# Kernel tuning notes

Hardware: AMD Instinct MI355X
Metric: run time of the kernel (lower is better)

The kernel has to match this reference:

```python
import jax, jax.numpy as jnp
import numpy as np

B, T, C = 8, 2048, 1024


def setup_inputs() -> dict:
    key = jax.random.key(0)
    ks = jax.random.split(key, 7)
    s = 0.02  # typical init scale for weights
    return {
        "x": jax.random.normal(ks[0], (B, T, C), jnp.float32),
        "wq": jax.random.normal(ks[1], (C, C), jnp.float32) * s,
        "bq": jax.random.normal(ks[2], (C,), jnp.float32) * s,
        "wk": jax.random.normal(ks[3], (C, C), jnp.float32) * s,
        "bk": jax.random.normal(ks[4], (C,), jnp.float32) * s,
        "wv": jax.random.normal(ks[5], (C, C), jnp.float32) * s,
        "bv": jax.random.normal(ks[6], (C,), jnp.float32) * s,
    }


def reference(x, wq, bq, wk, bk, wv, bv):
    # x: [B, T, C]; torch Linear stores weight as [out, in] -> x @ W.T + b
    Bx, Tx, Cx = x.shape
    Q = x @ wq.T + bq  # [B, T, C]
    K = x @ wk.T + bk
    V = x @ wv.T + bv
    # NOTE: source computes K @ Q^T (keys index rows, queries index columns)
    scores = jnp.einsum("btc,bsc->bts", K, Q) / jnp.sqrt(jnp.float32(Cx))  # [B, T, T]
    causal = jnp.tril(jnp.ones((Tx, Tx), dtype=bool))  # mask==0 above diagonal
    scores = jnp.where(causal, scores, -jnp.inf)
    # torch masked_fill with a (1,1,T,T) mask broadcasts scores to (1,B,T,T)
    scores = scores[None]  # [1, B, T, T]
    w = jax.nn.softmax(scores, axis=-1)
    out = jnp.einsum("abts,bsc->abtc", w, V)  # [1, B, T, C]
    return out
```

## Files before the change

### kernel.cpp

```cpp
#include <hip/hip_runtime.h>
#include <stdint.h>

typedef unsigned short u16;
typedef __attribute__((ext_vector_type(8))) __bf16 bf16x8;
typedef __attribute__((ext_vector_type(4))) float f32x4;

#define DEVI __device__ __forceinline__

DEVI u16 f32_to_bf16(float f) {
  uint32_t u = __builtin_bit_cast(uint32_t, f);
  u += 0x7FFFu + ((u >> 16) & 1u);
  return (u16)(u >> 16);
}

DEVI void gl2lds16(const void* g, void* l) {
  __builtin_amdgcn_global_load_lds(
      (const __attribute__((address_space(1))) void*)g,
      (__attribute__((address_space(3))) void*)l, 16, 0, 0);
}

#define SMEM_U16 17408

#define S_BATCH 2228224

DEVI void gemm_bt_mainloop(const u16* __restrict__ A, const u16* __restrict__ B,
                           int lda, int ldb, int kIters,
                           u16* As, u16* Bs, f32x4 (&acc)[4][4]) {
  const int tid = threadIdx.x;
  const int lane = tid & 63;
  const int wid = tid >> 6;
  const int wr = wid >> 1, wc = wid & 1;
  const int l15 = lane & 15, quad = lane >> 4;

  const int srow = tid >> 3;
  const int sgrp = ((tid & 7) - srow) & 7;
  const u16* Ag = A + (size_t)srow * lda + sgrp * 8;
  const u16* Bg = B + (size_t)srow * ldb + sgrp * 8;
  char* AsDst = (char*)As + tid * 16;
  char* BsDst = (char*)Bs + tid * 16;

  const int a_row0 = wr * 64 + l15;
  const int b_row0 = wc * 64 + l15;

  for (int kb = 0; kb < kIters; ++kb) {
#pragma unroll
    for (int r = 0; r < 4; ++r) {
      gl2lds16(Ag + (size_t)(r * 32) * lda, AsDst + r * 4096);
      gl2lds16(Bg + (size_t)(r * 32) * ldb, BsDst + r * 4096);
    }
    Ag += 64;
    Bg += 64;
    __syncthreads();
#pragma unroll
    for (int kk = 0; kk < 2; ++kk) {
      const int gA = ((kk * 4 + quad + a_row0) & 7) * 8;
      const int gB = ((kk * 4 + quad + b_row0) & 7) * 8;
      bf16x8 af[4], bfr[4];
#pragma unroll
      for (int i = 0; i < 4; ++i)
        af[i] = *(const bf16x8*)(As + (a_row0 + i * 16) * 64 + gA);
#pragma unroll
      for (int j = 0; j < 4; ++j)
        bfr[j] = *(const bf16x8*)(Bs + (b_row0 + j * 16) * 64 + gB);
#pragma unroll
      for (int i = 0; i < 4; ++i)
#pragma unroll
        for (int j = 0; j < 4; ++j)
          acc[i][j] = __builtin_amdgcn_mfma_f32_16x16x32_bf16(af[i], bfr[j],
                                                              acc[i][j], 0, 0, 0);
    }
    __syncthreads();
  }
}

DEVI void store_tile_bf16(const u16* tile, u16* __restrict__ out, int ld_out) {
  const int tid = threadIdx.x;
  const int c0 = (tid & 15) * 8;
#pragma unroll
  for (int rr = 0; rr < 8; ++rr) {
    const int row = rr * 16 + (tid >> 4);
    const uint4 v = *(const uint4*)(tile + row * 136 + c0);
    *(uint4*)(out + (size_t)row * ld_out + c0) = v;
  }
}

__global__ void cast_f32_to_bf16_kernel(const float* __restrict__ src,
                                        u16* __restrict__ dst, int n4) {
  int i = blockIdx.x * blockDim.x + threadIdx.x;
  const int stride = gridDim.x * blockDim.x;
  for (; i < n4; i += stride) {
    const float4 v = ((const float4*)src)[i];
    ushort4 o;
    o.x = f32_to_bf16(v.x);
    o.y = f32_to_bf16(v.y);
    o.z = f32_to_bf16(v.z);
    o.w = f32_to_bf16(v.w);
    ((ushort4*)dst)[i] = o;
  }
}

__global__ void cast_w_kernel(const float* __restrict__ wq,
                              const float* __restrict__ wk,
                              const float* __restrict__ wv,
                              u16* __restrict__ wb, float* __restrict__ sums) {
  const int z = blockIdx.y;
  if (z == 3) {
    int i = blockIdx.x * blockDim.x + threadIdx.x;
    if (i < 4096) ((float4*)sums)[i] = (float4){0.f, 0.f, 0.f, 0.f};
    return;
  }
  const float* src = (z == 0) ? wq : (z == 1) ? wk : wv;
  u16* dst = wb + (size_t)z * 1048576;
  int i = blockIdx.x * blockDim.x + threadIdx.x;
  const int stride = gridDim.x * blockDim.x;
  for (; i < 262144; i += stride) {
    const float4 v = ((const float4*)src)[i];
    ushort4 o;
    o.x = f32_to_bf16(v.x);
    o.y = f32_to_bf16(v.y);
    o.z = f32_to_bf16(v.z);
    o.w = f32_to_bf16(v.w);
    ((ushort4*)dst)[i] = o;
  }
}

__global__ __launch_bounds__(512, 2) void qkv_kernel(
    const u16* __restrict__ xb, const u16* __restrict__ wb,
    const float* __restrict__ bq, const float* __restrict__ bk,
    const float* __restrict__ bv, u16* __restrict__ Qb, u16* __restrict__ Kb,
    u16* __restrict__ Vt) {
  __shared__ __align__(16) u16 lds[65536];

  const int id = blockIdx.x;
  const int wg = (id & 7) * 96 + (id >> 3);
  const int g = wg >> 3, u = wg & 7;
  const int z = g >> 5;
  const int tp = g & 31;
  const int tmt = tp * 2 + (u >> 2);
  const int tct = u & 3;

  int m0, n0;
  const u16* Aptr;
  const u16* Bptr;
  if (z < 2) {
    m0 = tct * 256;
    n0 = tmt * 256;
    Aptr = wb + (size_t)z * 1048576 + (size_t)m0 * 1024;
    Bptr = xb + (size_t)n0 * 1024;
  } else {
    m0 = tmt * 256;
    n0 = tct * 256;
    Aptr = xb + (size_t)m0 * 1024;
    Bptr = wb + (size_t)2 * 1048576 + (size_t)n0 * 1024;
  }

  const int tid = threadIdx.x;
  const int srow = tid >> 3;
  const int sgrp = ((tid & 7) - srow) & 7;
  const u16* Ag = Aptr + (size_t)srow * 1024 + sgrp * 8;
  const u16* Bg = Bptr + (size_t)srow * 1024 + sgrp * 8;
  char* ldsDst = (char*)lds + tid * 16;

#define ST_A0(kt) do { const u16* s_ = Ag + (kt) * 64;           char* d_ = ldsDst + (((kt) & 1) * 65536);         gl2lds16(s_, d_); gl2lds16(s_ + 65536, d_ + 8192); } while (0)
#define ST_A1(kt) do { const u16* s_ = Ag + 131072 + (kt) * 64;  char* d_ = ldsDst + (((kt) & 1) * 65536) + 16384; gl2lds16(s_, d_); gl2lds16(s_ + 65536, d_ + 8192); } while (0)
#define ST_B0(kt) do { const u16* s_ = Bg + (kt) * 64;           char* d_ = ldsDst + (((kt) & 1) * 65536) + 32768; gl2lds16(s_, d_); gl2lds16(s_ + 65536, d_ + 8192); } while (0)
#define ST_B1(kt) do { const u16* s_ = Bg + 131072 + (kt) * 64;  char* d_ = ldsDst + (((kt) & 1) * 65536) + 49152; gl2lds16(s_, d_); gl2lds16(s_ + 65536, d_ + 8192); } while (0)

  ST_A0(0); ST_B0(0); ST_B1(0); ST_A1(0);
  ST_A0(1); ST_B0(1); ST_B1(1);

  const int lane = tid & 63, wid = tid >> 6;
  const int wr = wid >> 2, wc = wid & 3;
  const int l15 = lane & 15, quad = lane >> 4;

  int aoff[4][2], boff[2][2];
#pragma unroll
  for (int i_ = 0; i_ < 4; ++i_) {
    const int arow = wr * 64 + i_ * 16 + l15;
#pragma unroll
    for (int k_ = 0; k_ < 2; ++k_)
      aoff[i_][k_] = arow * 64 + ((k_ * 4 + quad + arow) & 7) * 8;
  }
#pragma unroll
  for (int j_ = 0; j_ < 2; ++j_) {
    const int brow = wc * 32 + j_ * 16 + l15;
#pragma unroll
    for (int k_ = 0; k_ < 2; ++k_)
      boff[j_][k_] = brow * 64 + ((k_ * 4 + quad + brow) & 7) * 8;
  }

  f32x4 acc[2][2][4][2];
#pragma unroll
  for (int a_ = 0; a_ < 2; ++a_)
#pragma unroll
    for (int b_ = 0; b_ < 2; ++b_)
#pragma unroll
      for (int i_ = 0; i_ < 4; ++i_)
#pragma unroll
        for (int j_ = 0; j_ < 2; ++j_)
          acc[a_][b_][i_][j_] = (f32x4){0.f, 0.f, 0.f, 0.f};

  bf16x8 af[4][2], bfr[2][2][2];

#define LOADA(qm, buf) do { const u16* p_ = lds + (buf) * 32768 + (qm) * 8192; \
  _Pragma("unroll") for (int i_ = 0; i_ < 4; ++i_) \
  _Pragma("unroll") for (int k_ = 0; k_ < 2; ++k_) \
    af[i_][k_] = *(const bf16x8*)(p_ + aoff[i_][k_]); } while (0)
#define LOADB(qn, buf) do { const u16* p_ = lds + (buf) * 32768 + 16384 + (qn) * 8192; \
  _Pragma("unroll") for (int j_ = 0; j_ < 2; ++j_) \
  _Pragma("unroll") for (int k_ = 0; k_ < 2; ++k_) \
    bfr[qn][j_][k_] = *(const bf16x8*)(p_ + boff[j_][k_]); } while (0)
#define MMA(qm, qn) do { \
  _Pragma("unroll") for (int i_ = 0; i_ < 4; ++i_) \
  _Pragma("unroll") for (int j_ = 0; j_ < 2; ++j_) \
  _Pragma("unroll") for (int k_ = 0; k_ < 2; ++k_) \
    acc[qm][qn][i_][j_] = __builtin_amdgcn_mfma_f32_16x16x32_bf16( \
        af[i_][k_], bfr[qn][j_][k_], acc[qm][qn][i_][j_], 0, 0, 0); } while (0)

#define BAR __builtin_amdgcn_s_barrier()
#define WLG0 asm volatile("s_waitcnt lgkmcnt(0)")
#define WLG8 asm volatile("s_waitcnt lgkmcnt(8)")
#define PRIO1 __builtin_amdgcn_s_setprio(1)
#define PRIO0 __builtin_amdgcn_s_setprio(0)

  asm volatile("s_waitcnt vmcnt(6)" ::: "memory");
  BAR;

#pragma unroll 1
  for (int it = 0; it < 7; ++it) {
    const int j0 = 2 * it;
    LOADA(0, 0); LOADB(0, 0); ST_A1(j0 + 1); WLG8;
    BAR; WLG0; PRIO1; MMA(0, 0); PRIO0; BAR;
    LOADB(1, 0); ST_A0(j0 + 2);
    BAR; WLG0; PRIO1; MMA(0, 1); PRIO0; BAR;
    LOADA(1, 0); ST_B0(j0 + 2);
    BAR; WLG0; PRIO1; MMA(1, 1); PRIO0; BAR;
    ST_B1(j0 + 2);
    BAR; PRIO1; MMA(1, 0); PRIO0;
    asm volatile("s_waitcnt vmcnt(6)" ::: "memory");
    BAR;
    LOADA(0, 1); LOADB(0, 1); ST_A1(j0 + 2); WLG8;
    BAR; WLG0; PRIO1; MMA(0, 0); PRIO0; BAR;
    LOADB(1, 1); ST_A0(j0 + 3);
    BAR; WLG0; PRIO1; MMA(0, 1); PRIO0; BAR;
    LOADA(1, 1); ST_B0(j0 + 3);
    BAR; WLG0; PRIO1; MMA(1, 1); PRIO0; BAR;
    ST_B1(j0 + 3);
    BAR; PRIO1; MMA(1, 0); PRIO0;
    asm volatile("s_waitcnt vmcnt(6)" ::: "memory");
    BAR;
  }
  {
    LOADA(0, 0); LOADB(0, 0); ST_A1(15); WLG8;
    BAR; WLG0; PRIO1; MMA(0, 0); PRIO0; BAR;
    LOADB(1, 0);
    BAR; WLG0; PRIO1; MMA(0, 1); PRIO0; BAR;
    LOADA(1, 0);
    BAR; WLG0; PRIO1; MMA(1, 1); PRIO0; BAR;
    PRIO1; MMA(1, 0); PRIO0;
    asm volatile("s_waitcnt vmcnt(0)" ::: "memory");
    BAR;
    LOADA(0, 1); LOADB(0, 1); WLG8;
    BAR; WLG0; PRIO1; MMA(0, 0); PRIO0; BAR;
    LOADB(1, 1);
    BAR; WLG0; PRIO1; MMA(0, 1); PRIO0; BAR;
    LOADA(1, 1);
    BAR; WLG0; PRIO1; MMA(1, 1); PRIO0; BAR;
    PRIO1; MMA(1, 0); PRIO0;
    BAR;
  }

  if (z < 2) {
    const float* bias = (z == 0) ? bq : bk;
    u16* Out = (z == 0) ? Qb : Kb;
#pragma unroll
    for (int th = 0; th < 2; ++th) {
      if (th) __syncthreads();
#pragma unroll
      for (int qm = 0; qm < 2; ++qm)
#pragma unroll
        for (int i_ = 0; i_ < 4; ++i_) {
          const int c = qm * 128 + wr * 64 + i_ * 16 + quad * 4;
          const float4 b4 = *(const float4*)(bias + m0 + c);
#pragma unroll
          for (int j_ = 0; j_ < 2; ++j_) {
            const int row = wc * 32 + j_ * 16 + l15;
            ushort4 o;
            o.x = f32_to_bf16(acc[qm][th][i_][j_][0] + b4.x);
            o.y = f32_to_bf16(acc[qm][th][i_][j_][1] + b4.y);
            o.z = f32_to_bf16(acc[qm][th][i_][j_][2] + b4.z);
            o.w = f32_to_bf16(acc[qm][th][i_][j_][3] + b4.w);
            *(ushort4*)(lds + row * 264 + c) = o;
          }
        }
      __syncthreads();
#pragma unroll
      for (int p = 0; p < 8; ++p) {
        const int row = p * 16 + (tid >> 5);
        const int c0 = (tid & 31) * 8;
        const uint4 v = *(const uint4*)(lds + row * 264 + c0);
        *(uint4*)(Out + (size_t)(n0 + th * 128 + row) * 1024 + m0 + c0) = v;
      }
    }
  } else {
    const int b = m0 >> 11;
    const int t0b = m0 & 2047;
    u16* Out = Vt + (size_t)b * 2097152;
#pragma unroll
    for (int th = 0; th < 2; ++th) {
      if (th) __syncthreads();
#pragma unroll
      for (int j_ = 0; j_ < 2; ++j_) {
        const int row = wc * 32 + j_ * 16 + l15;
        const float bb = bv[n0 + th * 128 + row];
#pragma unroll
        for (int qm = 0; qm < 2; ++qm)
#pragma unroll
          for (int i_ = 0; i_ < 4; ++i_) {
            const int c = qm * 128 + wr * 64 + i_ * 16 + quad * 4;
            ushort4 o;
            o.x = f32_to_bf16(acc[qm][th][i_][j_][0] + bb);
            o.y = f32_to_bf16(acc[qm][th][i_][j_][1] + bb);
            o.z = f32_to_bf16(acc[qm][th][i_][j_][2] + bb);
            o.w = f32_to_bf16(acc[qm][th][i_][j_][3] + bb);
            *(ushort4*)(lds + row * 264 + c) = o;
          }
      }
      __syncthreads();
#pragma unroll
      for (int p = 0; p < 8; ++p) {
        const int row = p * 16 + (tid >> 5);
        const int c0 = (tid & 31) * 8;
        const uint4 v = *(const uint4*)(lds + row * 264 + c0);
        *(uint4*)(Out + (size_t)(n0 + th * 128 + row) * 2048 + t0b + c0) = v;
      }
    }
  }
#undef ST_A0
#undef ST_A1
#undef ST_B0
#undef ST_B1
#undef LOADA
#undef LOADB
#undef MMA
#undef BAR
#undef WLG0
#undef WLG8
#undef PRIO1
#undef PRIO0
}

__global__ __launch_bounds__(256) void score_kernel(const u16* __restrict__ Kb,
                                                    const u16* __restrict__ Qb,
                                                    u16* __restrict__ Spk,
                                                    float* __restrict__ sums) {
  const int b = blockIdx.x & 7;
  const int l = 135 - (blockIdx.x >> 3);
  int rt = (int)((sqrtf(8.f * l + 1.f) - 1.f) * 0.5f);
  int ct = l - rt * (rt + 1) / 2;
  if (ct > rt) { ++rt; ct = l - rt * (rt + 1) / 2; }
  if (ct < 0)  { --rt; ct = l - rt * (rt + 1) / 2; }

  __shared__ __align__(16) u16 smem[SMEM_U16];
  u16* As = smem;
  u16* Bs = smem + 8192;

  f32x4 acc[4][4];
#pragma unroll
  for (int i = 0; i < 4; ++i)
#pragma unroll
    for (int j = 0; j < 4; ++j) acc[i][j] = (f32x4){0.f, 0.f, 0.f, 0.f};

  const u16* A = Qb + ((size_t)b * 2048 + ct * 128) * 1024;
  const u16* B = Kb + ((size_t)b * 2048 + rt * 128) * 1024;
  gemm_bt_mainloop(A, B, 1024, 1024, 16, As, Bs, acc);

  const int tid = threadIdx.x;
  const int lane = tid & 63, wid = tid >> 6;
  const int wr = wid >> 1, wc = wid & 1;
  const int l15 = lane & 15, quad = lane >> 4;
  const bool diag = (rt == ct);

  float sj[4] = {0.f, 0.f, 0.f, 0.f};
#pragma unroll
  for (int i = 0; i < 4; ++i) {
    const int s0 = wr * 64 + i * 16 + quad * 4;
#pragma unroll
    for (int j = 0; j < 4; ++j) {
      const int t = wc * 64 + j * 16 + l15;
      ushort4 o;
      float e[4];
#pragma unroll
      for (int r = 0; r < 4; ++r) {
        float v = __expf(acc[i][j][r] * 0.03125f);
        if (diag && (s0 + r) > t) v = 0.f;
        e[r] = v;
        sj[j] += v;
      }
      o.x = f32_to_bf16(e[0]);
      o.y = f32_to_bf16(e[1]);
      o.z = f32_to_bf16(e[2]);
      o.w = f32_to_bf16(e[3]);
      *(ushort4*)(smem + t * 136 + s0) = o;
    }
  }
#pragma unroll
  for (int j = 0; j < 4; ++j) {
    float v = sj[j];
    v += __shfl_xor(v, 16);
    v += __shfl_xor(v, 32);
    if (quad == 0)
      atomicAdd(&sums[(size_t)b * 2048 + rt * 128 + wc * 64 + j * 16 + l15], v);
  }
  __syncthreads();
  const int ld = (rt + 1) * 128;
  u16* Out = Spk + (size_t)b * S_BATCH + (size_t)(rt * (rt + 1) / 2) * 16384 +
             ct * 128;
  store_tile_bf16(smem, Out, ld);
}

__global__ __launch_bounds__(256) void pv_kernel(const u16* __restrict__ Spk,
                                                 const u16* __restrict__ Vt,
                                                 const float* __restrict__ sums,
                                                 float* __restrict__ Out) {
  const int b = blockIdx.x & 7;
  const int local = 127 - (blockIdx.x >> 3);
  const int rt = local >> 3;
  const int ct = local & 7;

  __shared__ __align__(16) u16 smem[SMEM_U16];
  u16* As = smem;
  u16* Bs = smem + 8192;
  float* ftile = (float*)smem;

  f32x4 acc[4][4];
#pragma unroll
  for (int i = 0; i < 4; ++i)
#pragma unroll
    for (int j = 0; j < 4; ++j) acc[i][j] = (f32x4){0.f, 0.f, 0.f, 0.f};

  const u16* A = Vt + ((size_t)b * 1024 + ct * 128) * 2048;
  const u16* B = Spk + (size_t)b * S_BATCH +
                 (size_t)(rt * (rt + 1) / 2) * 16384;
  const int ldb = (rt + 1) * 128;
  gemm_bt_mainloop(A, B, 2048, ldb, (rt + 1) * 2, As, Bs, acc);

  const int tid = threadIdx.x;
  const int lane = tid & 63, wid = tid >> 6;
  const int wr = wid >> 1, wc = wid & 1;
  const int l15 = lane & 15, quad = lane >> 4;

  const float* sumsb = sums + (size_t)b * 2048 + rt * 128;
  float* Ob = Out + (size_t)b * 2048 * 1024 + (size_t)(rt * 128) * 1024 +
              ct * 128;
#pragma unroll
  for (int h = 0; h < 2; ++h) {
    if (wc == h) {
#pragma unroll
      for (int j = 0; j < 4; ++j) {
        const int tl = j * 16 + l15;
        const float iv = 1.0f / sumsb[h * 64 + tl];
#pragma unroll
        for (int i = 0; i < 4; ++i) {
          const int c0 = wr * 64 + i * 16 + quad * 4;
          float4 v;
          v.x = acc[i][j][0] * iv;
          v.y = acc[i][j][1] * iv;
          v.z = acc[i][j][2] * iv;
          v.w = acc[i][j][3] * iv;
          *(float4*)(ftile + tl * 132 + c0) = v;
        }
      }
    }
    __syncthreads();
#pragma unroll
    for (int rr = 0; rr < 8; ++rr) {
      const int row = rr * 8 + (tid >> 5);
      const int c0 = (tid & 31) * 4;
      const float4 v = *(const float4*)(ftile + row * 132 + c0);
      *(float4*)(Ob + (size_t)(h * 64 + row) * 1024 + c0) = v;
    }
    __syncthreads();
  }
}

extern "C" void kernel_launch(void* const* d_in, const int* in_sizes, int n_in,
                              void* d_out, int out_size, void* d_ws,
                              size_t ws_size, hipStream_t stream) {
  const float* x = (const float*)d_in[0];
  const float* wq = (const float*)d_in[1];
  const float* bq = (const float*)d_in[2];
  const float* wk = (const float*)d_in[3];
  const float* bk = (const float*)d_in[4];
  const float* wv = (const float*)d_in[5];
  const float* bv = (const float*)d_in[6];
  float* out = (float*)d_out;
  char* ws = (char*)d_ws;

  u16* Qb = (u16*)(ws);
  u16* Kb = (u16*)(ws + ((size_t)32 << 20));
  u16* Vt = (u16*)(ws + ((size_t)64 << 20));
  u16* Spk = (u16*)(ws + ((size_t)96 << 20));
  u16* xb = (u16*)(ws + ((size_t)96 << 20));
  float* sums = (float*)(ws + ((size_t)132 << 20));
  u16* wb = (u16*)(ws + ((size_t)134 << 20));

  cast_f32_to_bf16_kernel<<<16384, 256, 0, stream>>>(x, xb, 16777216 / 4);
  cast_w_kernel<<<dim3(512, 4), 256, 0, stream>>>(wq, wk, wv, wb, sums);

  qkv_kernel<<<768, 512, 0, stream>>>(xb, wb, bq, bk, bv, Qb, Kb, Vt);

  score_kernel<<<8 * 136, 256, 0, stream>>>(Kb, Qb, Spk, sums);

  pv_kernel<<<8 * 128, 256, 0, stream>>>(Spk, Vt, sums, out);
}
```

Before: 337.7 us.

## Rewrite score kernel with 256x128 tiles and pipelined LDS loads

The score kernel moves from 128x128 tiles with 256 threads to 256x128 tiles (256 query rows by 128 key rows) with 512 threads. It reuses the qkv kernel's double-buffered global_load_lds pipeline with setprio and interleaved barriers, and the tile enumeration is remapped so that diagonal tiles are half-masked. The qkv mainloop also reorders its LDS fragment loads to run right after each MMA phase instead of before the barrier, dropping the partial lgkmcnt waits. The aim is better operand reuse and fewer blocks for the score GEMM. The cost is that partially masked half tiles still compute their full 256 columns, and the larger LDS footprint lowers occupancy.

```diff
diff --git a/kernel.cpp b/kernel.cpp
--- a/kernel.cpp
+++ b/kernel.cpp
@@ -70,17 +70,6 @@
                                                               acc[i][j], 0, 0, 0);
     }
     __syncthreads();
-  }
-}
-
-DEVI void store_tile_bf16(const u16* tile, u16* __restrict__ out, int ld_out) {
-  const int tid = threadIdx.x;
-  const int c0 = (tid & 15) * 8;
-#pragma unroll
-  for (int rr = 0; rr < 8; ++rr) {
-    const int row = rr * 16 + (tid >> 4);
-    const uint4 v = *(const uint4*)(tile + row * 136 + c0);
-    *(uint4*)(out + (size_t)row * ld_out + c0) = v;
   }
 }
 
@@ -219,55 +208,51 @@
 
 #define BAR __builtin_amdgcn_s_barrier()
 #define WLG0 asm volatile("s_waitcnt lgkmcnt(0)")
-#define WLG8 asm volatile("s_waitcnt lgkmcnt(8)")
 #define PRIO1 __builtin_amdgcn_s_setprio(1)
 #define PRIO0 __builtin_amdgcn_s_setprio(0)
-
-  asm volatile("s_waitcnt vmcnt(6)" ::: "memory");
+#define WVM6 asm volatile("s_waitcnt vmcnt(6)" ::: "memory")
+#define WVM0 asm volatile("s_waitcnt vmcnt(0)" ::: "memory")
+
+  WVM6;
   BAR;
 
 #pragma unroll 1
   for (int it = 0; it < 7; ++it) {
     const int j0 = 2 * it;
-    LOADA(0, 0); LOADB(0, 0); ST_A1(j0 + 1); WLG8;
-    BAR; WLG0; PRIO1; MMA(0, 0); PRIO0; BAR;
-    LOADB(1, 0); ST_A0(j0 + 2);
-    BAR; WLG0; PRIO1; MMA(0, 1); PRIO0; BAR;
-    LOADA(1, 0); ST_B0(j0 + 2);
+    LOADA(0, 0); LOADB(0, 0); ST_A1(j0 + 1);
+    BAR; WLG0; PRIO1; MMA(0, 0); PRIO0; LOADB(1, 0); BAR;
+    ST_A0(j0 + 2);
+    BAR; WLG0; PRIO1; MMA(0, 1); PRIO0; LOADA(1, 0); BAR;
+    ST_B0(j0 + 2);
     BAR; WLG0; PRIO1; MMA(1, 1); PRIO0; BAR;
     ST_B1(j0 + 2);
     BAR; PRIO1; MMA(1, 0); PRIO0;
-    asm volatile("s_waitcnt vmcnt(6)" ::: "memory");
+    WVM6;
     BAR;
-    LOADA(0, 1); LOADB(0, 1); ST_A1(j0 + 2); WLG8;
-    BAR; WLG0; PRIO1; MMA(0, 0); PRIO0; BAR;
-    LOADB(1, 1); ST_A0(j0 + 3);
-    BAR; WLG0; PRIO1; MMA(0, 1); PRIO0; BAR;
-    LOADA(1, 1); ST_B0(j0 + 3);
+    LOADA(0, 1); LOADB(0, 1); ST_A1(j0 + 2);
+    BAR; WLG0; PRIO1; MMA(0, 0); PRIO0; LOADB(1, 1); BAR;
+    ST_A0(j0 + 3);
+    BAR; WLG0; PRIO1; MMA(0, 1); PRIO0; LOADA(1, 1); BAR;
+    ST_B0(j0 + 3);
     BAR; WLG0; PRIO1; MMA(1, 1); PRIO0; BAR;
     ST_B1(j0 + 3);
     BAR; PRIO1; MMA(1, 0); PRIO0;
-    asm volatile("s_waitcnt vmcnt(6)" ::: "memory");
+    WVM6;
     BAR;
   }
   {
-    LOADA(0, 0); LOADB(0, 0); ST_A1(15); WLG8;
-    BAR; WLG0; PRIO1; MMA(0, 0); PRIO0; BAR;
-    LOADB(1, 0);
-    BAR; WLG0; PRIO1; MMA(0, 1); PRIO0; BAR;
-    LOADA(1, 0);
+    LOADA(0, 0); LOADB(0, 0); ST_A1(15);
+    BAR; WLG0; PRIO1; MMA(0, 0); PRIO0; LOADB(1, 0); BAR;
+    BAR; WLG0; PRIO1; MMA(0, 1); PRIO0; LOADA(1, 0); BAR;
+    BAR; WLG0; PRIO1; MMA(1, 1); PRIO0; BAR;
+    BAR; PRIO1; MMA(1, 0); PRIO0;
+    WVM0;
+    BAR;
+    LOADA(0, 1); LOADB(0, 1);
+    BAR; WLG0; PRIO1; MMA(0, 0); PRIO0; LOADB(1, 1); BAR;
+    BAR; WLG0; PRIO1; MMA(0, 1); PRIO0; LOADA(1, 1); BAR;
     BAR; WLG0; PRIO1; MMA(1, 1); PRIO0; BAR;
     PRIO1; MMA(1, 0); PRIO0;
-    asm volatile("s_waitcnt vmcnt(0)" ::: "memory");
-    BAR;
-    LOADA(0, 1); LOADB(0, 1); WLG8;
-    BAR; WLG0; PRIO1; MMA(0, 0); PRIO0; BAR;
-    LOADB(1, 1);
-    BAR; WLG0; PRIO1; MMA(0, 1); PRIO0; BAR;
-    LOADA(1, 1);
-    BAR; WLG0; PRIO1; MMA(1, 1); PRIO0; BAR;
-    PRIO1; MMA(1, 0); PRIO0;
-    BAR;
   }
 
   if (z < 2) {
@@ -345,78 +330,197 @@
 #undef MMA
 #undef BAR
 #undef WLG0
-#undef WLG8
 #undef PRIO1
 #undef PRIO0
-}
-
-__global__ __launch_bounds__(256) void score_kernel(const u16* __restrict__ Kb,
-                                                    const u16* __restrict__ Qb,
-                                                    u16* __restrict__ Spk,
-                                                    float* __restrict__ sums) {
-  const int b = blockIdx.x & 7;
-  const int l = 135 - (blockIdx.x >> 3);
-  int rt = (int)((sqrtf(8.f * l + 1.f) - 1.f) * 0.5f);
-  int ct = l - rt * (rt + 1) / 2;
-  if (ct > rt) { ++rt; ct = l - rt * (rt + 1) / 2; }
-  if (ct < 0)  { --rt; ct = l - rt * (rt + 1) / 2; }
-
-  __shared__ __align__(16) u16 smem[SMEM_U16];
-  u16* As = smem;
-  u16* Bs = smem + 8192;
-
-  f32x4 acc[4][4];
-#pragma unroll
-  for (int i = 0; i < 4; ++i)
-#pragma unroll
-    for (int j = 0; j < 4; ++j) acc[i][j] = (f32x4){0.f, 0.f, 0.f, 0.f};
-
-  const u16* A = Qb + ((size_t)b * 2048 + ct * 128) * 1024;
+#undef WVM6
+#undef WVM0
+}
+
+__global__ __launch_bounds__(512, 2) void score_kernel(const u16* __restrict__ Kb,
+                                                       const u16* __restrict__ Qb,
+                                                       u16* __restrict__ Spk,
+                                                       float* __restrict__ sums) {
+  __shared__ __align__(16) u16 lds[49152];
+
+  const int id = blockIdx.x;
+  const int b = id & 7;
+  const int l = id >> 3;
+  int k = (int)((sqrtf(4.f * l + 1.f) - 1.f) * 0.5f);
+  if (k * (k + 1) > l) --k;
+  if ((k + 1) * (k + 2) <= l) ++k;
+  const int off = l - k * (k + 1);
+  const int hi = (off >= (k + 1));
+  const int rt = 2 * k + hi;
+  const int ct = off - (hi ? (k + 1) : 0);
+  const bool maskT = (ct == k);
+
+  const int tid = threadIdx.x;
+  const int srow = tid >> 3;
+  const int sgrp = ((tid & 7) - srow) & 7;
+  const u16* A = Qb + ((size_t)b * 2048 + ct * 256) * 1024;
   const u16* B = Kb + ((size_t)b * 2048 + rt * 128) * 1024;
-  gemm_bt_mainloop(A, B, 1024, 1024, 16, As, Bs, acc);
-
-  const int tid = threadIdx.x;
+  const u16* Ag = A + (size_t)srow * 1024 + sgrp * 8;
+  const u16* Bg = B + (size_t)srow * 1024 + sgrp * 8;
+  char* ldsDst = (char*)lds + tid * 16;
+
+#define ST_A0(kt) do { const u16* s_ = Ag + (kt) * 64;           char* d_ = ldsDst + (((kt) & 1) * 49152);         gl2lds16(s_, d_); gl2lds16(s_ + 65536, d_ + 8192); } while (0)
+#define ST_A1(kt) do { const u16* s_ = Ag + 131072 + (kt) * 64;  char* d_ = ldsDst + (((kt) & 1) * 49152) + 16384; gl2lds16(s_, d_); gl2lds16(s_ + 65536, d_ + 8192); } while (0)
+#define ST_B(kt)  do { const u16* s_ = Bg + (kt) * 64;           char* d_ = ldsDst + (((kt) & 1) * 49152) + 32768; gl2lds16(s_, d_); gl2lds16(s_ + 65536, d_ + 8192); } while (0)
+
+  ST_A0(0); ST_B(0); ST_A1(0);
+  ST_A0(1); ST_B(1);
+
   const int lane = tid & 63, wid = tid >> 6;
-  const int wr = wid >> 1, wc = wid & 1;
+  const int wr = wid >> 2, wc = wid & 3;
   const int l15 = lane & 15, quad = lane >> 4;
-  const bool diag = (rt == ct);
-
-  float sj[4] = {0.f, 0.f, 0.f, 0.f};
-#pragma unroll
-  for (int i = 0; i < 4; ++i) {
-    const int s0 = wr * 64 + i * 16 + quad * 4;
-#pragma unroll
-    for (int j = 0; j < 4; ++j) {
-      const int t = wc * 64 + j * 16 + l15;
-      ushort4 o;
-      float e[4];
-#pragma unroll
-      for (int r = 0; r < 4; ++r) {
-        float v = __expf(acc[i][j][r] * 0.03125f);
-        if (diag && (s0 + r) > t) v = 0.f;
-        e[r] = v;
-        sj[j] += v;
+
+  int aoff[4][2], boff[2][2];
+#pragma unroll
+  for (int i_ = 0; i_ < 4; ++i_) {
+    const int arow = wr * 64 + i_ * 16 + l15;
+#pragma unroll
+    for (int k_ = 0; k_ < 2; ++k_)
+      aoff[i_][k_] = arow * 64 + ((k_ * 4 + quad + arow) & 7) * 8;
+  }
+#pragma unroll
+  for (int j_ = 0; j_ < 2; ++j_) {
+    const int brow = wc * 32 + j_ * 16 + l15;
+#pragma unroll
+    for (int k_ = 0; k_ < 2; ++k_)
+      boff[j_][k_] = brow * 64 + ((k_ * 4 + quad + brow) & 7) * 8;
+  }
+
+  f32x4 acc[2][4][2];
+#pragma unroll
+  for (int q_ = 0; q_ < 2; ++q_)
+#pragma unroll
+    for (int i_ = 0; i_ < 4; ++i_)
+#pragma unroll
+      for (int j_ = 0; j_ < 2; ++j_)
+        acc[q_][i_][j_] = (f32x4){0.f, 0.f, 0.f, 0.f};
+
+  bf16x8 af[4][2], bfr[2][2];
+
+#define SLOADA(qm, buf) do { const u16* p_ = lds + (buf) * 24576 + (qm) * 8192; \
+  _Pragma("unroll") for (int i_ = 0; i_ < 4; ++i_) \
+  _Pragma("unroll") for (int k_ = 0; k_ < 2; ++k_) \
+    af[i_][k_] = *(const bf16x8*)(p_ + aoff[i_][k_]); } while (0)
+#define SLOADB(buf) do { const u16* p_ = lds + (buf) * 24576 + 16384; \
+  _Pragma("unroll") for (int j_ = 0; j_ < 2; ++j_) \
+  _Pragma("unroll") for (int k_ = 0; k_ < 2; ++k_) \
+    bfr[j_][k_] = *(const bf16x8*)(p_ + boff[j_][k_]); } while (0)
+#define SMMA(qm) do { \
+  _Pragma("unroll") for (int i_ = 0; i_ < 4; ++i_) \
+  _Pragma("unroll") for (int j_ = 0; j_ < 2; ++j_) \
+  _Pragma("unroll") for (int k_ = 0; k_ < 2; ++k_) \
+    acc[qm][i_][j_] = __builtin_amdgcn_mfma_f32_16x16x32_bf16( \
+        af[i_][k_], bfr[j_][k_], acc[qm][i_][j_], 0, 0, 0); } while (0)
+
+#define BAR __builtin_amdgcn_s_barrier()
+#define WLG0 asm volatile("s_waitcnt lgkmcnt(0)")
+#define PRIO1 __builtin_amdgcn_s_setprio(1)
+#define PRIO0 __builtin_amdgcn_s_setprio(0)
+#define WVM4 asm volatile("s_waitcnt vmcnt(4)" ::: "memory")
+#define WVM0 asm volatile("s_waitcnt vmcnt(0)" ::: "memory")
+
+  WVM4;
+  BAR;
+
+#pragma unroll 1
+  for (int it = 0; it < 7; ++it) {
+    const int j0 = 2 * it;
+    SLOADA(0, 0); SLOADB(0); ST_A1(j0 + 1);
+    BAR; WLG0; PRIO1; SMMA(0); PRIO0; SLOADA(1, 0); BAR;
+    ST_A0(j0 + 2); ST_B(j0 + 2);
+    BAR; WLG0; PRIO1; SMMA(1); PRIO0;
+    WVM4;
+    BAR;
+    SLOADA(0, 1); SLOADB(1); ST_A1(j0 + 2);
+    BAR; WLG0; PRIO1; SMMA(0); PRIO0; SLOADA(1, 1); BAR;
+    ST_A0(j0 + 3); ST_B(j0 + 3);
+    BAR; WLG0; PRIO1; SMMA(1); PRIO0;
+    WVM4;
+    BAR;
+  }
+  {
+    SLOADA(0, 0); SLOADB(0); ST_A1(15);
+    BAR; WLG0; PRIO1; SMMA(0); PRIO0; SLOADA(1, 0); BAR;
+    BAR; WLG0; PRIO1; SMMA(1); PRIO0;
+    WVM0;
+    BAR;
+    SLOADA(0, 1); SLOADB(1);
+    BAR; WLG0; PRIO1; SMMA(0); PRIO0; SLOADA(1, 1); BAR;
+    BAR; WLG0; PRIO1; SMMA(1); PRIO0; BAR;
+  }
+
+  const int moff = (rt & 1) * 128;
+  float sj[2] = {0.f, 0.f};
+#pragma unroll
+  for (int qm = 0; qm < 2; ++qm)
+#pragma unroll
+    for (int i_ = 0; i_ < 4; ++i_) {
+      const int s0 = qm * 128 + wr * 64 + i_ * 16 + quad * 4;
+#pragma unroll
+      for (int j_ = 0; j_ < 2; ++j_) {
+        const int t = wc * 32 + j_ * 16 + l15;
+        ushort4 o;
+        float e[4];
+#pragma unroll
+        for (int r = 0; r < 4; ++r) {
+          float v = __expf(acc[qm][i_][j_][r] * 0.03125f);
+          if (maskT && (s0 + r) > (t + moff)) v = 0.f;
+          e[r] = v;
+          sj[j_] += v;
+        }
+        o.x = f32_to_bf16(e[0]);
+        o.y = f32_to_bf16(e[1]);
+        o.z = f32_to_bf16(e[2]);
+        o.w = f32_to_bf16(e[3]);
+        *(ushort4*)(lds + t * 264 + s0) = o;
       }
-      o.x = f32_to_bf16(e[0]);
-      o.y = f32_to_bf16(e[1]);
-      o.z = f32_to_bf16(e[2]);
-      o.w = f32_to_bf16(e[3]);
-      *(ushort4*)(smem + t * 136 + s0) = o;
-    }
-  }
-#pragma unroll
-  for (int j = 0; j < 4; ++j) {
-    float v = sj[j];
+    }
+#pragma unroll
+  for (int j_ = 0; j_ < 2; ++j_) {
+    float v = sj[j_];
     v += __shfl_xor(v, 16);
     v += __shfl_xor(v, 32);
     if (quad == 0)
-      atomicAdd(&sums[(size_t)b * 2048 + rt * 128 + wc * 64 + j * 16 + l15], v);
+      atomicAdd(&sums[(size_t)b * 2048 + rt * 128 + wc * 32 + j_ * 16 + l15], v);
   }
   __syncthreads();
   const int ld = (rt + 1) * 128;
+  const int nc = ld - ct * 256;
   u16* Out = Spk + (size_t)b * S_BATCH + (size_t)(rt * (rt + 1) / 2) * 16384 +
-             ct * 128;
-  store_tile_bf16(smem, Out, ld);
+             ct * 256;
+  if (nc >= 256) {
+#pragma unroll
+    for (int p = 0; p < 8; ++p) {
+      const int row = p * 16 + (tid >> 5);
+      const int c0 = (tid & 31) * 8;
+      const uint4 v = *(const uint4*)(lds + row * 264 + c0);
+      *(uint4*)(Out + (size_t)row * ld + c0) = v;
+    }
+  } else {
+#pragma unroll
+    for (int p = 0; p < 4; ++p) {
+      const int row = p * 32 + (tid >> 4);
+      const int c0 = (tid & 15) * 8;
+      const uint4 v = *(const uint4*)(lds + row * 264 + c0);
+      *(uint4*)(Out + (size_t)row * ld + c0) = v;
+    }
+  }
+#undef ST_A0
+#undef ST_A1
+#undef ST_B
+#undef SLOADA
+#undef SLOADB
+#undef SMMA
+#undef BAR
+#undef WLG0
+#undef PRIO1
+#undef PRIO0
+#undef WVM4
+#undef WVM0
 }
 
 __global__ __launch_bounds__(256) void pv_kernel(const u16* __restrict__ Spk,
@@ -510,7 +614,7 @@
 
   qkv_kernel<<<768, 512, 0, stream>>>(xb, wb, bq, bk, bv, Qb, Kb, Vt);
 
-  score_kernel<<<8 * 136, 256, 0, stream>>>(Kb, Qb, Spk, sums);
+  score_kernel<<<576, 512, 0, stream>>>(Kb, Qb, Spk, sums);
 
   pv_kernel<<<8 * 128, 256, 0, stream>>>(Spk, Vt, sums, out);
 }
```

Result: no change. 333.3 us (-1.3%).
